# Kernel tuning notes

Hardware: AMD Instinct MI355X
Metric: run time of the kernel (lower is better)

Reference implementation:

```python
import jax, jax.numpy as jnp
import numpy as np

N = 1_048_576   # flattened tokens
C = 128         # classes
IGNORE = 0
GAMMA = 1.0     # FocalLoss bug: alpha default (1) becomes self.gamma
BETA = 1.0      # ClassficationAndMDCA: self.beta = alpha = 1.0


def setup_inputs() -> dict:
    key = jax.random.key(0)
    k1, k2 = jax.random.split(key)
    inputs = jax.random.normal(k1, (N, C), dtype=jnp.float32)
    targets = jax.random.randint(k2, (N,), 0, C, dtype=jnp.int64)
    return {"inputs": inputs, "targets": targets}


def reference(inputs, targets):
    # ignore_index filtering expressed as masked reductions (jit-friendly)
    mask = (targets != IGNORE)
    maskf = mask.astype(inputs.dtype)               # [N]
    nvalid = jnp.sum(maskf)

    # Focal loss: -(1-pt)^gamma * log pt, mean over valid tokens
    logp = jax.nn.log_softmax(inputs, axis=1)       # [N, C]
    logpt = jnp.take_along_axis(logp, targets[:, None], axis=1)[:, 0]  # [N]
    pt = jnp.exp(logpt)
    focal = -((1.0 - pt) ** GAMMA) * logpt
    loss_cls = jnp.sum(focal * maskf) / nvalid

    # MDCA: per-class |mean confidence - mean label frequency|, mean over classes
    probs = jnp.exp(logp)                           # softmax, reuse log_softmax
    avg_conf = jnp.sum(probs * maskf[:, None], axis=0) / nvalid        # [C]
    avg_count = jnp.zeros((C,), inputs.dtype).at[targets].add(maskf) / nvalid  # [C]
    loss_cal = jnp.mean(jnp.abs(avg_conf - avg_count))

    return loss_cls + BETA * loss_cal
```

## Files before the change

### kernel.cpp

```cpp
#include <hip/hip_runtime.h>

#define NC 128
#define BLOCK 256
#define GRID 2048

__global__ void cmdca_init(float* __restrict__ acc) {
    int i = threadIdx.x;
    if (i < 2 * NC + 2) acc[i] = 0.0f;
}

template <int CTRL>
__device__ __forceinline__ float dpp_add(float v) {
    int s = __builtin_amdgcn_update_dpp(0, __float_as_int(v), CTRL, 0xF, 0xF, true);
    return v + __int_as_float(s);
}

__device__ __forceinline__ float half_sum_dpp(float v) {
    v = dpp_add<0x111>(v);
    v = dpp_add<0x112>(v);
    v = dpp_add<0x114>(v);
    v = dpp_add<0x118>(v);
    v = dpp_add<0x142>(v);
    return v;
}

__global__ __launch_bounds__(BLOCK) void cmdca_main(const float* __restrict__ in,
                                                    const int* __restrict__ tgt,
                                                    float* __restrict__ acc,
                                                    int nrows) {
    const int lane  = threadIdx.x & 63;
    const int l31   = lane & 31;
    const int half  = lane >> 5;
    const int wave  = blockIdx.x * (BLOCK >> 6) + (threadIdx.x >> 6);
    const int nwaves = GRID * (BLOCK >> 6);

    float conf0 = 0.f, conf1 = 0.f, conf2 = 0.f, conf3 = 0.f;
    float cnt0  = 0.f, cnt1  = 0.f, cnt2  = 0.f, cnt3  = 0.f;
    float focal = 0.f, nval  = 0.f;

    auto load = [&](int pair, float4& x, int& t, int& ok) {
        int myrow = pair * 2 + half;
        ok = (myrow < nrows);
        int r = ok ? myrow : (nrows - 1);
        x = *reinterpret_cast<const float4*>(in + (size_t)r * NC + l31 * 4);
        t = tgt[r];
    };

    auto compute = [&](const float4& x, int t, int ok) {
        float e0 = __expf(x.x), e1 = __expf(x.y), e2 = __expf(x.z), e3 = __expf(x.w);
        float sv = half_sum_dpp((e0 + e1) + (e2 + e3));
        float s_lo = __int_as_float(__builtin_amdgcn_readlane(__float_as_int(sv), 31));
        float s_hi = __int_as_float(__builtin_amdgcn_readlane(__float_as_int(sv), 63));
        float s = half ? s_hi : s_lo;
        float invs = 1.0f / s;
        float logZ = __logf(s);
        int te = t & 3;
        float xsel = (te == 0) ? x.x : (te == 1) ? x.y : (te == 2) ? x.z : x.w;
        int t_lo = __builtin_amdgcn_readlane(t, 0);
        int t_hi = __builtin_amdgcn_readlane(t, 32);
        float xt_lo = __int_as_float(
            __builtin_amdgcn_readlane(__float_as_int(xsel), t_lo >> 2));
        float xt_hi = __int_as_float(
            __builtin_amdgcn_readlane(__float_as_int(xsel), 32 + (t_hi >> 2)));
        float xt = half ? xt_hi : xt_lo;
        float logpt = xt - logZ;
        float pt = __expf(logpt);
        float valid = (t != 0 && ok) ? 1.0f : 0.0f;
        nval  += valid;
        focal += valid * (-(1.0f - pt) * logpt);
        float vs = valid * invs;
        conf0 += vs * e0; conf1 += vs * e1; conf2 += vs * e2; conf3 += vs * e3;
        float inc = (l31 == (t >> 2)) ? valid : 0.f;
        cnt0 += (te == 0) ? inc : 0.f;
        cnt1 += (te == 1) ? inc : 0.f;
        cnt2 += (te == 2) ? inc : 0.f;
        cnt3 += (te == 3) ? inc : 0.f;
    };

    const int npairs = (nrows + 1) >> 1;
    int p = wave;
    for (; p + 3 * nwaves < npairs; p += 4 * nwaves) {
        float4 x0, x1, x2, x3; int t0, t1, t2, t3, o0, o1, o2, o3;
        load(p,              x0, t0, o0);
        load(p + nwaves,     x1, t1, o1);
        load(p + 2 * nwaves, x2, t2, o2);
        load(p + 3 * nwaves, x3, t3, o3);
        compute(x0, t0, o0);
        compute(x1, t1, o1);
        compute(x2, t2, o2);
        compute(x3, t3, o3);
    }
    for (; p < npairs; p += nwaves) {
        float4 x; int t, ok;
        load(p, x, t, ok);
        compute(x, t, ok);
    }

    __shared__ float sconf[NC];
    __shared__ float scnt[NC];
    __shared__ float sfn[2];
    if (threadIdx.x < NC) { sconf[threadIdx.x] = 0.f; scnt[threadIdx.x] = 0.f; }
    if (threadIdx.x < 2)  sfn[threadIdx.x] = 0.f;
    __syncthreads();
    int cb = 4 * l31;
    atomicAdd(&sconf[cb + 0], conf0);
    atomicAdd(&sconf[cb + 1], conf1);
    atomicAdd(&sconf[cb + 2], conf2);
    atomicAdd(&sconf[cb + 3], conf3);
    atomicAdd(&scnt[cb + 0], cnt0);
    atomicAdd(&scnt[cb + 1], cnt1);
    atomicAdd(&scnt[cb + 2], cnt2);
    atomicAdd(&scnt[cb + 3], cnt3);
    if (l31 == 0) {
        atomicAdd(&sfn[0], focal);
        atomicAdd(&sfn[1], nval);
    }
    __syncthreads();
    if (threadIdx.x < NC) {
        atomicAdd(&acc[threadIdx.x],      sconf[threadIdx.x]);
        atomicAdd(&acc[NC + threadIdx.x], scnt[threadIdx.x]);
    }
    if (threadIdx.x == 0) {
        atomicAdd(&acc[2 * NC],     sfn[0]);
        atomicAdd(&acc[2 * NC + 1], sfn[1]);
    }
}

__global__ void cmdca_fin(const float* __restrict__ acc, float* __restrict__ out) {
    int c = threadIdx.x;
    float nvalid = acc[2 * NC + 1];
    float diff = fabsf(acc[c] - acc[NC + c]) / nvalid;
    #pragma unroll
    for (int o = 32; o; o >>= 1) diff += __shfl_xor(diff, o);
    __shared__ float sh[2];
    if ((threadIdx.x & 63) == 0) sh[threadIdx.x >> 6] = diff;
    __syncthreads();
    if (threadIdx.x == 0) {
        float loss_cal = (sh[0] + sh[1]) / (float)NC;
        float loss_cls = acc[2 * NC] / nvalid;
        out[0] = loss_cls + loss_cal;
    }
}

extern "C" void kernel_launch(void* const* d_in, const int* in_sizes, int n_in,
                              void* d_out, int out_size, void* d_ws, size_t ws_size,
                              hipStream_t stream) {
    const float* in  = (const float*)d_in[0];
    const int*   tgt = (const int*)d_in[1];
    float* out = (float*)d_out;
    float* acc = (float*)d_ws;
    int nrows = in_sizes[0] / NC;

    hipLaunchKernelGGL(cmdca_init, dim3(1), dim3(512), 0, stream, acc);
    hipLaunchKernelGGL(cmdca_main, dim3(GRID), dim3(BLOCK), 0, stream, in, tgt, acc, nrows);
    hipLaunchKernelGGL(cmdca_fin,  dim3(1), dim3(NC), 0, stream, acc, out);
}
```

Baseline: 135.3 us.

## Use contiguous per-wave chunks, nontemporal loads, and fuse finalize via last-block pattern

Each wave now processes a contiguous chunk of row pairs instead of a grid-strided set, using a two-deep software-pipelined load/compute loop. Input and target reads are nontemporal. Grid and block sizes change to 512x1024, and the divide becomes a hardware reciprocal. The separate finalize kernel is removed: a last-block-done counter lets the final block compute the loss, which saves one launch at the cost of a threadfence and an atomic counter.

```diff
diff --git a/kernel.cpp b/kernel.cpp
--- a/kernel.cpp
+++ b/kernel.cpp
@@ -1,12 +1,14 @@
 #include <hip/hip_runtime.h>
 
 #define NC 128
-#define BLOCK 256
-#define GRID 2048
+#define BLOCK 1024
+#define GRID  512
+
+typedef float f32x4 __attribute__((ext_vector_type(4)));
 
 __global__ void cmdca_init(float* __restrict__ acc) {
     int i = threadIdx.x;
-    if (i < 2 * NC + 2) acc[i] = 0.0f;
+    if (i < 260) acc[i] = 0.0f;
 }
 
 template <int CTRL>
@@ -14,7 +16,6 @@
     int s = __builtin_amdgcn_update_dpp(0, __float_as_int(v), CTRL, 0xF, 0xF, true);
     return v + __int_as_float(s);
 }
-
 __device__ __forceinline__ float half_sum_dpp(float v) {
     v = dpp_add<0x111>(v);
     v = dpp_add<0x112>(v);
@@ -24,81 +25,88 @@
     return v;
 }
 
-__global__ __launch_bounds__(BLOCK) void cmdca_main(const float* __restrict__ in,
-                                                    const int* __restrict__ tgt,
-                                                    float* __restrict__ acc,
-                                                    int nrows) {
-    const int lane  = threadIdx.x & 63;
-    const int l31   = lane & 31;
-    const int half  = lane >> 5;
-    const int wave  = blockIdx.x * (BLOCK >> 6) + (threadIdx.x >> 6);
+__global__ __launch_bounds__(BLOCK, 8) void cmdca_main(const float* __restrict__ in,
+                                                       const int* __restrict__ tgt,
+                                                       float* __restrict__ acc,
+                                                       float* __restrict__ out,
+                                                       int nrows) {
+    const int lane = threadIdx.x & 63;
+    const int l31  = lane & 31;
+    const int half = lane >> 5;
+    const int wave = blockIdx.x * (BLOCK >> 6) + (threadIdx.x >> 6);
     const int nwaves = GRID * (BLOCK >> 6);
+    const int npairs = (nrows + 1) >> 1;
+    const int ppw = (npairs + nwaves - 1) / nwaves;
 
     float conf0 = 0.f, conf1 = 0.f, conf2 = 0.f, conf3 = 0.f;
-    float cnt0  = 0.f, cnt1  = 0.f, cnt2  = 0.f, cnt3  = 0.f;
-    float focal = 0.f, nval  = 0.f;
+    float cnt0 = 0.f, cnt1 = 0.f, cnt2 = 0.f, cnt3 = 0.f;
+    float focal = 0.f, nval = 0.f;
 
-    auto load = [&](int pair, float4& x, int& t, int& ok) {
-        int myrow = pair * 2 + half;
-        ok = (myrow < nrows);
-        int r = ok ? myrow : (nrows - 1);
-        x = *reinterpret_cast<const float4*>(in + (size_t)r * NC + l31 * 4);
-        t = tgt[r];
+    auto load = [&](int pp, f32x4& x, int& t) {
+        int row = min(2 * pp + half, nrows - 1);
+        x = __builtin_nontemporal_load(
+                reinterpret_cast<const f32x4*>(in + (size_t)row * NC + l31 * 4));
+        t = __builtin_nontemporal_load(tgt + row);
     };
 
-    auto compute = [&](const float4& x, int t, int ok) {
+    auto compute = [&](const f32x4 x, int t, int row0) {
         float e0 = __expf(x.x), e1 = __expf(x.y), e2 = __expf(x.z), e3 = __expf(x.w);
         float sv = half_sum_dpp((e0 + e1) + (e2 + e3));
-        float s_lo = __int_as_float(__builtin_amdgcn_readlane(__float_as_int(sv), 31));
-        float s_hi = __int_as_float(__builtin_amdgcn_readlane(__float_as_int(sv), 63));
-        float s = half ? s_hi : s_lo;
-        float invs = 1.0f / s;
+        float s0 = __int_as_float(__builtin_amdgcn_readlane(__float_as_int(sv), 31));
+        float s1 = __int_as_float(__builtin_amdgcn_readlane(__float_as_int(sv), 63));
+        float s  = half ? s1 : s0;
+        float invs = __builtin_amdgcn_rcpf(s);
         float logZ = __logf(s);
-        int te = t & 3;
+        int te = t & 3, tq = t >> 2;
         float xsel = (te == 0) ? x.x : (te == 1) ? x.y : (te == 2) ? x.z : x.w;
-        int t_lo = __builtin_amdgcn_readlane(t, 0);
-        int t_hi = __builtin_amdgcn_readlane(t, 32);
-        float xt_lo = __int_as_float(
-            __builtin_amdgcn_readlane(__float_as_int(xsel), t_lo >> 2));
-        float xt_hi = __int_as_float(
-            __builtin_amdgcn_readlane(__float_as_int(xsel), 32 + (t_hi >> 2)));
-        float xt = half ? xt_hi : xt_lo;
+        int tlo = __builtin_amdgcn_readlane(t, 0);
+        int thi = __builtin_amdgcn_readlane(t, 32);
+        float xt0 = __int_as_float(
+            __builtin_amdgcn_readlane(__float_as_int(xsel), tlo >> 2));
+        float xt1 = __int_as_float(
+            __builtin_amdgcn_readlane(__float_as_int(xsel), 32 + (thi >> 2)));
+        float xt = half ? xt1 : xt0;
         float logpt = xt - logZ;
         float pt = __expf(logpt);
-        float valid = (t != 0 && ok) ? 1.0f : 0.0f;
+        float valid = (t != 0) ? 1.0f : 0.0f;
+        valid = (row0 + half < nrows) ? valid : 0.0f;
         nval  += valid;
-        focal += valid * (-(1.0f - pt) * logpt);
+        focal += valid * (pt - 1.0f) * logpt;
         float vs = valid * invs;
         conf0 += vs * e0; conf1 += vs * e1; conf2 += vs * e2; conf3 += vs * e3;
-        float inc = (l31 == (t >> 2)) ? valid : 0.f;
+        float inc = (l31 == tq) ? valid : 0.f;
         cnt0 += (te == 0) ? inc : 0.f;
         cnt1 += (te == 1) ? inc : 0.f;
         cnt2 += (te == 2) ? inc : 0.f;
         cnt3 += (te == 3) ? inc : 0.f;
     };
 
-    const int npairs = (nrows + 1) >> 1;
-    int p = wave;
-    for (; p + 3 * nwaves < npairs; p += 4 * nwaves) {
-        float4 x0, x1, x2, x3; int t0, t1, t2, t3, o0, o1, o2, o3;
-        load(p,              x0, t0, o0);
-        load(p + nwaves,     x1, t1, o1);
-        load(p + 2 * nwaves, x2, t2, o2);
-        load(p + 3 * nwaves, x3, t3, o3);
-        compute(x0, t0, o0);
-        compute(x1, t1, o1);
-        compute(x2, t2, o2);
-        compute(x3, t3, o3);
-    }
-    for (; p < npairs; p += nwaves) {
-        float4 x; int t, ok;
-        load(p, x, t, ok);
-        compute(x, t, ok);
+    int p   = wave * ppw;
+    int end = min(p + ppw, npairs);
+    if (p < end) {
+        f32x4 xA; int tA;
+        load(p, xA, tA);
+        for (; p + 2 < end; p += 2) {
+            f32x4 xB; int tB;
+            load(p + 1, xB, tB);
+            compute(xA, tA, 2 * p);
+            load(p + 2, xA, tA);
+            compute(xB, tB, 2 * (p + 1));
+        }
+        if (p + 1 < end) {
+            f32x4 xB; int tB;
+            load(p + 1, xB, tB);
+            compute(xA, tA, 2 * p);
+            compute(xB, tB, 2 * (p + 1));
+        } else {
+            compute(xA, tA, 2 * p);
+        }
     }
 
     __shared__ float sconf[NC];
     __shared__ float scnt[NC];
     __shared__ float sfn[2];
+    __shared__ int slast;
     if (threadIdx.x < NC) { sconf[threadIdx.x] = 0.f; scnt[threadIdx.x] = 0.f; }
     if (threadIdx.x < 2)  sfn[threadIdx.x] = 0.f;
     __syncthreads();
@@ -124,21 +132,28 @@
         atomicAdd(&acc[2 * NC],     sfn[0]);
         atomicAdd(&acc[2 * NC + 1], sfn[1]);
     }
-}
 
-__global__ void cmdca_fin(const float* __restrict__ acc, float* __restrict__ out) {
-    int c = threadIdx.x;
-    float nvalid = acc[2 * NC + 1];
-    float diff = fabsf(acc[c] - acc[NC + c]) / nvalid;
-    #pragma unroll
-    for (int o = 32; o; o >>= 1) diff += __shfl_xor(diff, o);
-    __shared__ float sh[2];
-    if ((threadIdx.x & 63) == 0) sh[threadIdx.x >> 6] = diff;
+    __threadfence();
     __syncthreads();
     if (threadIdx.x == 0) {
-        float loss_cal = (sh[0] + sh[1]) / (float)NC;
-        float loss_cls = acc[2 * NC] / nvalid;
-        out[0] = loss_cls + loss_cal;
+        unsigned old = atomicAdd(reinterpret_cast<unsigned*>(&acc[258]), 1u);
+        slast = (old == (unsigned)(gridDim.x - 1));
+    }
+    __syncthreads();
+    if (slast) {
+        if (threadIdx.x < NC) {
+            float c = atomicAdd(&acc[threadIdx.x], 0.f);
+            float k = atomicAdd(&acc[NC + threadIdx.x], 0.f);
+            sconf[threadIdx.x] = fabsf(c - k);
+        }
+        __syncthreads();
+        if (threadIdx.x == 0) {
+            float fo = atomicAdd(&acc[2 * NC], 0.f);
+            float nv = atomicAdd(&acc[2 * NC + 1], 0.f);
+            float sum = 0.f;
+            for (int i = 0; i < NC; ++i) sum += sconf[i];
+            out[0] = fo / nv + sum / (nv * (float)NC);
+        }
     }
 }
 
@@ -152,6 +167,6 @@
     int nrows = in_sizes[0] / NC;
 
     hipLaunchKernelGGL(cmdca_init, dim3(1), dim3(512), 0, stream, acc);
-    hipLaunchKernelGGL(cmdca_main, dim3(GRID), dim3(BLOCK), 0, stream, in, tgt, acc, nrows);
-    hipLaunchKernelGGL(cmdca_fin,  dim3(1), dim3(NC), 0, stream, acc, out);
+    hipLaunchKernelGGL(cmdca_main, dim3(GRID), dim3(BLOCK), 0, stream,
+                       in, tgt, acc, out, nrows);
 }
```

New measurement: 254.2 us. 1.88x slower.
